# Kernel optimization log

Measured on AMD Instinct MI355X. Metric: run time of the kernel, lower is better.

Reference implementation:

```python
import jax, jax.numpy as jnp
import numpy as np

B, N, D, H = 8, 577, 768, 12
HD = D // H
SCALE = HD ** -0.5
LN_EPS = 1e-5


def layer_norm(x, w, b):
    mu = jnp.mean(x, -1, keepdims=True)
    var = jnp.mean((x - mu) ** 2, -1, keepdims=True)
    return (x - mu) * jax.lax.rsqrt(var + LN_EPS) * w + b


def wasserstein_distance_matmul(mean1, cov1, mean2, cov2):
    # all [B,H,N,hd]; returns [B,H,N,N]
    m1_2 = jnp.sum(mean1 ** 2, -1, keepdims=True)
    m2_2 = jnp.sum(mean2 ** 2, -1, keepdims=True)
    ret = -2.0 * jnp.einsum('bhnd,bhmd->bhnm', mean1, mean2) + m1_2 + jnp.swapaxes(m2_2, -1, -2)
    c1s = jnp.sqrt(jnp.clip(cov1, 1e-24))
    c2s = jnp.sqrt(jnp.clip(cov2, 1e-24))
    cov_ret = (-2.0 * jnp.einsum('bhnd,bhmd->bhnm', c1s, c2s)
               + jnp.sum(cov1, -1, keepdims=True)
               + jnp.swapaxes(jnp.sum(cov2, -1, keepdims=True), -1, -2))
    return ret + cov_ret


def setup_inputs() -> dict:
    key = jax.random.key(0)
    ks = jax.random.split(key, 20)
    s = 0.02
    return {
        'x_mean': jax.random.normal(ks[0], (B, N, D), jnp.float32),
        'x_cov': jax.random.normal(ks[1], (B, N, D), jnp.float32),
        'rel_pos_bias': jax.random.normal(ks[2], (1, H, N, N), jnp.float32),
        'norm1_w': jnp.ones((D,), jnp.float32),
        'norm1_b': jnp.zeros((D,), jnp.float32),
        'qkv_w': jax.random.normal(ks[3], (3 * D, D), jnp.float32) * s,
        'proj_w': jax.random.normal(ks[4], (D, D), jnp.float32) * s,
        'proj_b': jnp.zeros((D,), jnp.float32),
        'cov_proj_w': jax.random.normal(ks[5], (D, D), jnp.float32) * s,
        'cov_proj_b': jnp.zeros((D,), jnp.float32),
        'norm2_w': jnp.ones((D,), jnp.float32),
        'norm2_b': jnp.zeros((D,), jnp.float32),
        'fc1_w': jax.random.normal(ks[6], (4 * D, D), jnp.float32) * s,
        'fc1_b': jnp.zeros((4 * D,), jnp.float32),
        'fc2_w': jax.random.normal(ks[7], (D, 4 * D), jnp.float32) * s,
        'fc2_b': jnp.zeros((D,), jnp.float32),
        'gamma1': 0.1 * jnp.ones((D,), jnp.float32),
        'gamma2': 0.1 * jnp.ones((D,), jnp.float32),
    }


def _split_heads(t):
    # [B,N,3D] -> q,k,v each [B,H,N,hd]
    t = t.reshape(B, N, 3, H, HD).transpose(2, 0, 3, 1, 4)
    return t[0], t[1], t[2]


def attention(xm, xc, rel_pos_bias, qkv_w, proj_w, proj_b, cov_proj_w, cov_proj_b):
    qkv = xm @ qkv_w.T                                  # [B,N,3D]
    q, k, v = _split_heads(qkv)
    cov_qkv = jax.nn.elu(xc @ qkv_w.T) + 1.0            # same weights for cov stream
    cov_q, cov_k, cov_v = _split_heads(cov_qkv)
    q = q * SCALE
    attn = -wasserstein_distance_matmul(q, cov_q, k, cov_k)
    attn = jax.nn.sigmoid(attn + 1e-24)
    attn = jax.nn.softmax(attn + rel_pos_bias, axis=-1)  # [B,H,N,N]
    mean_ctx = jnp.einsum('bhnm,bhmd->bhnd', attn, v).transpose(0, 2, 1, 3).reshape(B, N, D)
    cov_ctx = jnp.einsum('bhnm,bhmd->bhnd', attn ** 2, cov_v).transpose(0, 2, 1, 3).reshape(B, N, D)
    mean_out = mean_ctx @ proj_w.T + proj_b
    cov_out = cov_ctx @ cov_proj_w.T + cov_proj_b
    return mean_out, cov_out


def mlp(x, fc1_w, fc1_b, fc2_w, fc2_b):
    h = jax.nn.gelu(x @ fc1_w.T + fc1_b, approximate=False)
    return h @ fc2_w.T + fc2_b


def reference(x_mean, x_cov, rel_pos_bias, norm1_w, norm1_b, qkv_w, proj_w, proj_b,
              cov_proj_w, cov_proj_b, norm2_w, norm2_b, fc1_w, fc1_b, fc2_w, fc2_b,
              gamma1, gamma2):
    mean, cov = attention(layer_norm(x_mean, norm1_w, norm1_b),
                          layer_norm(x_cov, norm1_w, norm1_b),
                          rel_pos_bias, qkv_w, proj_w, proj_b, cov_proj_w, cov_proj_b)
    x_mean = x_mean + gamma1 * mean
    fcm = gamma2 * mlp(layer_norm(x_mean, norm2_w, norm2_b), fc1_w, fc1_b, fc2_w, fc2_b)
    x_cov = x_cov + gamma1 * cov
    fcc = gamma2 * mlp(layer_norm(x_cov, norm2_w, norm2_b), fc1_w, fc1_b, fc2_w, fc2_b)
    return (x_mean + fcm, x_cov + fcc)
```

## Files before the change

kernel.cpp:

```cpp
#include <hip/hip_runtime.h>
#include <hip/hip_bf16.h>
#include <math.h>
#include <stdint.h>

typedef __bf16 bf16;
typedef __attribute__((ext_vector_type(8))) __bf16 bf16x8;
typedef __attribute__((ext_vector_type(4))) float f32x4;

typedef __attribute__((address_space(1))) void gas_void;
typedef __attribute__((address_space(3))) void las_void;

#define DEV __device__ __forceinline__

static constexpr int B_ = 8, N_ = 577, D_ = 768, H_ = 12;
static constexpr int M_ = B_ * N_;
static constexpr int MP_ = 4736;
static constexpr int NP_ = 640;
static constexpr int BH_ = B_ * H_;
static constexpr float SCALE_ = 0.125f;

DEV void async_cp16(const void* g, void* l) {
  __builtin_amdgcn_global_load_lds((gas_void*)g, (las_void*)l, 16, 0, 0);
}
DEV float fast_rcp(float x) { return __builtin_amdgcn_rcpf(x); }
DEV float elu1(float x) { return x > 0.0f ? x + 1.0f : __expf(x); }
DEV float fast_gelu(float x) {
  const float x2 = x * x;
  const float z = x * fmaf(0.0713548826f, x2, 1.5957691216f);
  return x * fast_rcp(1.0f + __expf(-z));
}

__global__ __launch_bounds__(256) void cvt6_kernel(
    const float* __restrict__ s0, const float* __restrict__ s1,
    const float* __restrict__ s2, const float* __restrict__ s3,
    const float* __restrict__ s4, const float* __restrict__ s5,
    bf16* __restrict__ d0, bf16* __restrict__ d1, bf16* __restrict__ d2,
    bf16* __restrict__ d3, bf16* __restrict__ d4, bf16* __restrict__ d5,
    int n0, int n1, int n2, int n3, int n4c, int n5) {
  const float* ss[6] = {s0, s1, s2, s3, s4, s5};
  bf16* dd[6] = {d0, d1, d2, d3, d4, d5};
  const int nn[6] = {n0, n1, n2, n3, n4c, n5};
  int bid = blockIdx.x;
  int seg = 0;
#pragma unroll 6
  for (int k = 0; k < 6; k++) {
    const int nb = (nn[k] + 255) >> 8;
    if (bid < nb) { seg = k; break; }
    bid -= nb;
  }
  const int i = bid * 256 + threadIdx.x;
  if (i < nn[seg]) {
    const float4 v = ((const float4*)ss[seg])[i];
    bf16 o[4] = {(bf16)v.x, (bf16)v.y, (bf16)v.z, (bf16)v.w};
    *(uint64_t*)(dd[seg] + (size_t)i * 4) = *(const uint64_t*)o;
  }
}

__global__ __launch_bounds__(256) void ln2_kernel(
    const float* __restrict__ x0, const float* __restrict__ x1,
    const float* __restrict__ w, const float* __restrict__ bp,
    bf16* __restrict__ out) {
  const int row = blockIdx.x;
  const int st = (int)(row >= M_);
  const int srow = row - st * M_;
  const float* xr = (st ? x1 : x0) + (size_t)srow * D_;
  const int t = threadIdx.x;
  float v0 = xr[t], v1 = xr[t + 256], v2 = xr[t + 512];
  float s = v0 + v1 + v2;
  float ss = v0 * v0 + v1 * v1 + v2 * v2;
#pragma unroll
  for (int m = 32; m >= 1; m >>= 1) {
    s += __shfl_down(s, m);
    ss += __shfl_down(ss, m);
  }
  __shared__ float red[8];
  if ((t & 63) == 0) { red[t >> 6] = s; red[4 + (t >> 6)] = ss; }
  __syncthreads();
  s = red[0] + red[1] + red[2] + red[3];
  ss = red[4] + red[5] + red[6] + red[7];
  const float mu = s * (1.0f / D_);
  float var = ss * (1.0f / D_) - mu * mu;
  var = fmaxf(var, 0.0f);
  const float rs = rsqrtf(var + 1e-5f);
  bf16* orow = out + ((size_t)st * MP_ + srow) * D_;
  orow[t]       = (bf16)((v0 - mu) * rs * w[t]       + bp[t]);
  orow[t + 256] = (bf16)((v1 - mu) * rs * w[t + 256] + bp[t + 256]);
  orow[t + 512] = (bf16)((v2 - mu) * rs * w[t + 512] + bp[t + 512]);
}

enum { EP_BF16 = 0, EP_PROJ = 1, EP_GELU = 2, EP_FC2 = 3 };

template <int EP, int K>
__global__ __launch_bounds__(256) void gemm_bt(
    const bf16* __restrict__ A, const bf16* __restrict__ W0,
    const bf16* __restrict__ W1, int Nn, int gx,
    const float* __restrict__ bias0, const float* __restrict__ bias1,
    const float* __restrict__ gamma,
    const float* __restrict__ resid0, const float* __restrict__ resid1,
    bf16* __restrict__ Cb, float* __restrict__ Cf0, float* __restrict__ Cf1) {
  __shared__ __align__(16) bf16 As[3][128 * 32];
  __shared__ __align__(16) bf16 Bs[3][128 * 32];
  const int nwg = gridDim.x;
  const int o = blockIdx.x;
  const int q = nwg >> 3, r = nwg & 7, xcd = o & 7;
  const int flat = (xcd < r ? xcd * (q + 1) : r * (q + 1) + (xcd - r) * q) + (o >> 3);
  const int bx = flat % gx, by = flat / gx;

  const int t = threadIdx.x;
  const int lane = t & 63, wv = t >> 6;
  const int ln = lane & 15, kg = lane >> 4;
  const int wr = wv >> 1, wc = wv & 1;
  const int s = (int)(by >= (MP_ / 128));
  const bf16* W = s ? W1 : W0;
  const size_t brow = (size_t)by * 128;
  const size_t bcol = (size_t)bx * 128;
  const int r0 = t >> 2, gsl = t & 3;
  const bf16* A0 = A + (brow + r0) * (size_t)K + gsl * 8;
  const bf16* A1 = A + (brow + r0 + 64) * (size_t)K + gsl * 8;
  const bf16* W0p = W + (bcol + r0) * (size_t)K + gsl * 8;
  const bf16* W1p = W + (bcol + r0 + 64) * (size_t)K + gsl * 8;

  auto stage = [&](int buf, int kk) {
    async_cp16(A0 + kk, &As[buf][(wv * 64) * 8]);
    async_cp16(A1 + kk, &As[buf][(256 + wv * 64) * 8]);
    async_cp16(W0p + kk, &Bs[buf][(wv * 64) * 8]);
    async_cp16(W1p + kk, &Bs[buf][(256 + wv * 64) * 8]);
  };

  f32x4 acc[4][4] = {};
  constexpr int nt = K >> 5;
  static_assert(nt % 3 == 0, "K/32 must be divisible by 3");
  stage(0, 0);
  stage(1, 32);
#pragma unroll 1
  for (int tb = 0; tb < nt; tb += 3) {
#pragma unroll
    for (int u = 0; u < 3; u++) {
      const int tt = tb + u;
      if (tt + 1 < nt) {
        asm volatile("s_waitcnt vmcnt(4)" ::: "memory");
      } else {
        asm volatile("s_waitcnt vmcnt(0)" ::: "memory");
      }
      __builtin_amdgcn_s_barrier();
      bf16x8 af[4], bfr[4];
#pragma unroll
      for (int i = 0; i < 4; i++)
        af[i] = *(const bf16x8*)&As[u][(wr * 64 + i * 16 + ln) * 32 + kg * 8];
#pragma unroll
      for (int j = 0; j < 4; j++)
        bfr[j] = *(const bf16x8*)&Bs[u][(wc * 64 + j * 16 + ln) * 32 + kg * 8];
#pragma unroll
      for (int i = 0; i < 4; i++)
#pragma unroll
        for (int j = 0; j < 4; j++)
          acc[i][j] = __builtin_amdgcn_mfma_f32_16x16x32_bf16(af[i], bfr[j], acc[i][j], 0, 0, 0);
      if (tt + 2 < nt) stage((u + 2) % 3, (tt + 2) * 32);
    }
  }

  const float* biasS = s ? bias1 : bias0;
  const float* residS = s ? resid1 : resid0;
  float* CfS = s ? Cf1 : Cf0;
#pragma unroll
  for (int i = 0; i < 4; i++) {
    const int rb = (int)brow + wr * 64 + i * 16 + kg * 4;
#pragma unroll
    for (int j = 0; j < 4; j++) {
      const int col = (int)bcol + wc * 64 + j * 16 + ln;
#pragma unroll
      for (int rr = 0; rr < 4; rr++) {
        const int row = rb + rr;
        float v = acc[i][j][rr];
        if (EP == EP_BF16) {
          Cb[(size_t)row * Nn + col] = (bf16)v;
        } else if (EP == EP_GELU) {
          v += biasS[col];
          Cb[(size_t)row * Nn + col] = (bf16)fast_gelu(v);
        } else {
          const int r2 = row - s * MP_;
          if (r2 < M_) {
            v += biasS[col];
            if (EP == EP_PROJ) {
              CfS[(size_t)r2 * Nn + col] = residS[(size_t)r2 * Nn + col] + gamma[col] * v;
            } else {
              CfS[(size_t)r2 * Nn + col] += gamma[col] * v;
            }
          }
        }
      }
    }
  }
}

__global__ __launch_bounds__(256) void prep_kernel(
    const bf16* __restrict__ qm, const bf16* __restrict__ qc,
    bf16* __restrict__ Qcat, bf16* __restrict__ Kcat,
    bf16* __restrict__ Vt, bf16* __restrict__ CVt,
    float* __restrict__ rowt, float* __restrict__ colt) {
  const int n0 = blockIdx.x * 64;
  const int h = blockIdx.y, b = blockIdx.z;
  const int bh = b * H_ + h;
  const int t = threadIdx.x;
  const int nl = t >> 2, c = t & 3;
  const int n = n0 + nl;
  const bool valid = n < N_;
  __shared__ bf16 vts[64][72], cvts[64][72];
  float q2 = 0.f, cqs = 0.f, k2 = 0.f, cks = 0.f;
  bf16 qo[16], sqo[16], ko[16], sko[16];
  if (valid) {
    const size_t ro = (size_t)(b * N_ + n) * 2304 + h * 64 + c * 16;
#pragma unroll
    for (int half = 0; half < 2; half++) {
      bf16x8 qv8 = *(const bf16x8*)(qm + ro + half * 8);
      bf16x8 kv8 = *(const bf16x8*)(qm + ro + 768 + half * 8);
      bf16x8 vv8 = *(const bf16x8*)(qm + ro + 1536 + half * 8);
      bf16x8 cq8 = *(const bf16x8*)(qc + ro + half * 8);
      bf16x8 ck8 = *(const bf16x8*)(qc + ro + 768 + half * 8);
      bf16x8 cv8 = *(const bf16x8*)(qc + ro + 1536 + half * 8);
#pragma unroll
      for (int i = 0; i < 8; i++) {
        const int d = half * 8 + i;
        float qv = (float)qv8[i] * SCALE_;
        float kv = (float)kv8[i];
        float cq1 = elu1((float)cq8[i]);
        float ck1 = elu1((float)ck8[i]);
        q2 += qv * qv; cqs += cq1; k2 += kv * kv; cks += ck1;
        qo[d] = (bf16)qv; sqo[d] = (bf16)sqrtf(fmaxf(cq1, 1e-24f));
        ko[d] = (bf16)kv; sko[d] = (bf16)sqrtf(fmaxf(ck1, 1e-24f));
        vts[nl][c * 16 + d] = vv8[i];
        cvts[nl][c * 16 + d] = (bf16)elu1((float)cv8[i]);
      }
    }
  } else {
#pragma unroll
    for (int d = 0; d < 16; d++) {
      qo[d] = (bf16)0.f; sqo[d] = (bf16)0.f; ko[d] = (bf16)0.f; sko[d] = (bf16)0.f;
      vts[nl][c * 16 + d] = (bf16)0.f; cvts[nl][c * 16 + d] = (bf16)0.f;
    }
  }
  {
    bf16* qrow = Qcat + ((size_t)bh * NP_ + n) * 128;
    bf16* krow = Kcat + ((size_t)bh * NP_ + n) * 128;
#pragma unroll
    for (int d = 0; d < 16; d++) {
      qrow[c * 16 + d] = qo[d];
      qrow[64 + c * 16 + d] = sqo[d];
      krow[c * 16 + d] = ko[d];
      krow[64 + c * 16 + d] = sko[d];
    }
  }
  float rt = q2 + cqs, ct = k2 + cks;
  rt += __shfl_xor(rt, 1); rt += __shfl_xor(rt, 2);
  ct += __shfl_xor(ct, 1); ct += __shfl_xor(ct, 2);
  if (c == 0) { rowt[(size_t)bh * NP_ + n] = rt; colt[(size_t)bh * NP_ + n] = ct; }
  __syncthreads();
  const int drow = t >> 2;
  const size_t vb = ((size_t)bh * 64 + drow) * NP_ + n0 + c * 16;
#pragma unroll
  for (int i = 0; i < 16; i++) {
    Vt[vb + i] = vts[c * 16 + i][drow];
    CVt[vb + i] = cvts[c * 16 + i][drow];
  }
}

__global__ __launch_bounds__(256) void attn_kernel(
    const bf16* __restrict__ Qcat, const bf16* __restrict__ Kcat,
    const bf16* __restrict__ Vt, const bf16* __restrict__ CVt,
    const float* __restrict__ rowt, const float* __restrict__ colt,
    const bf16* __restrict__ bias,
    bf16* __restrict__ ctxm, bf16* __restrict__ ctxc) {
  const int id = blockIdx.x;
  const int xcd = id & 7, slot = id >> 3;
  const int g = xcd + 8 * (slot / 10);
  const int it = slot % 10;
  const int b = g / H_, h = g % H_;
  const int bh = g;
  const int i0 = it * 64;
  const int t = threadIdx.x;
  const int lane = t & 63, w = t >> 6;
  const int ln = lane & 15, kg = lane >> 4;
  __shared__ __align__(16) bf16 Ks[64 * 128];
  __shared__ __align__(16) bf16 Vs[64 * 64];
  __shared__ __align__(16) bf16 CVs[64 * 64];
  __shared__ __align__(16) bf16 Ps[64 * 72];

  const bf16* Qg = Qcat + (size_t)bh * NP_ * 128;
  const bf16* Kg = Kcat + (size_t)bh * NP_ * 128;
  const bf16* Vg = Vt + (size_t)bh * 64 * NP_;
  const bf16* CVg = CVt + (size_t)bh * 64 * NP_;

#pragma unroll
  for (int qq = 0; qq < 4; qq++) {
    const int idx = qq * 256 + t;
    const int row = idx >> 4, sl = idx & 15;
    async_cp16(Qg + (size_t)(i0 + row) * 128 + ((sl ^ (row & 7)) * 8),
               &Ks[(qq * 256 + w * 64) * 8]);
  }
  __syncthreads();
  bf16x8 aq[4];
  {
    const int row = w * 16 + ln;
#pragma unroll
    for (int kc = 0; kc < 4; kc++) {
      const int slot2 = kc * 4 + kg;
      aq[kc] = *(const bf16x8*)&Ks[row * 128 + ((slot2 ^ (row & 7)) * 8)];
    }
  }
  float rt[4];
#pragma unroll
  for (int r = 0; r < 4; r++) rt[r] = rowt[(size_t)bh * NP_ + i0 + w * 16 + kg * 4 + r];

  f32x4 accm[4] = {}, accc[4] = {};
  float den[4] = {0.f, 0.f, 0.f, 0.f};
  const int igb = i0 + w * 16 + kg * 4;

  for (int jt = 0; jt < 10; jt++) {
    const int j0 = jt * 64;
    __syncthreads();
#pragma unroll
    for (int qq = 0; qq < 4; qq++) {
      const int idx = qq * 256 + t;
      const int row = idx >> 4, sl = idx & 15;
      async_cp16(Kg + (size_t)(j0 + row) * 128 + ((sl ^ (row & 7)) * 8),
                 &Ks[(qq * 256 + w * 64) * 8]);
    }
#pragma unroll
    for (int qq = 0; qq < 2; qq++) {
      const int idx = qq * 256 + t;
      const int row = idx >> 3, sl = idx & 7;
      async_cp16(Vg + (size_t)row * NP_ + j0 + ((sl ^ (row & 7)) * 8),
                 &Vs[(qq * 256 + w * 64) * 8]);
      async_cp16(CVg + (size_t)row * NP_ + j0 + ((sl ^ (row & 7)) * 8),
                 &CVs[(qq * 256 + w * 64) * 8]);
    }
    float bb[4][4], ctb[4];
#pragma unroll
    for (int js = 0; js < 4; js++) {
      const int jg = j0 + js * 16 + ln;
      const int jc = jg < N_ ? jg : N_ - 1;
      ctb[js] = colt[(size_t)bh * NP_ + jg];
#pragma unroll
      for (int r = 0; r < 4; r++) {
        const int ic = (igb + r) < N_ ? (igb + r) : N_ - 1;
        bb[js][r] = (float)bias[((size_t)h * N_ + ic) * N_ + jc];
      }
    }
    __syncthreads();
#pragma unroll
    for (int js = 0; js < 4; js++) {
      f32x4 sv = {};
#pragma unroll
      for (int kc = 0; kc < 4; kc++) {
        const int row = js * 16 + ln;
        const int slot2 = kc * 4 + kg;
        bf16x8 bk = *(const bf16x8*)&Ks[row * 128 + ((slot2 ^ (row & 7)) * 8)];
        sv = __builtin_amdgcn_mfma_f32_16x16x32_bf16(aq[kc], bk, sv, 0, 0, 0);
      }
      const int jg = j0 + js * 16 + ln;
#pragma unroll
      for (int r = 0; r < 4; r++) {
        const float S = 2.0f * sv[r] - rt[r] - ctb[js];
        const float sig = fast_rcp(1.0f + __expf(-S));
        float e = __expf(sig + bb[js][r]);
        if (jg >= N_) e = 0.0f;
        const bf16 eb = (bf16)e;
        den[r] += (float)eb;
        Ps[(w * 16 + kg * 4 + r) * 72 + js * 16 + ln] = eb;
      }
    }
#pragma unroll
    for (int ks = 0; ks < 2; ks++) {
      const int prow = w * 16 + ln;
      bf16x8 pa = *(const bf16x8*)&Ps[prow * 72 + ks * 32 + kg * 8];
      bf16x8 p2a;
#pragma unroll
      for (int i = 0; i < 8; i++) {
        const float pf = (float)pa[i];
        p2a[i] = (bf16)(pf * pf);
      }
#pragma unroll
      for (int nt = 0; nt < 4; nt++) {
        const int vrow = nt * 16 + ln;
        const int slot2 = ks * 4 + kg;
        bf16x8 vb = *(const bf16x8*)&Vs[vrow * 64 + ((slot2 ^ (vrow & 7)) * 8)];
        bf16x8 cvb = *(const bf16x8*)&CVs[vrow * 64 + ((slot2 ^ (vrow & 7)) * 8)];
        accm[nt] = __builtin_amdgcn_mfma_f32_16x16x32_bf16(pa, vb, accm[nt], 0, 0, 0);
        accc[nt] = __builtin_amdgcn_mfma_f32_16x16x32_bf16(p2a, cvb, accc[nt], 0, 0, 0);
      }
    }
  }
#pragma unroll
  for (int r = 0; r < 4; r++) {
    float d = den[r];
    d += __shfl_xor(d, 1); d += __shfl_xor(d, 2);
    d += __shfl_xor(d, 4); d += __shfl_xor(d, 8);
    den[r] = d;
  }
#pragma unroll
  for (int r = 0; r < 4; r++) {
    const int ig = i0 + w * 16 + kg * 4 + r;
    if (ig < N_) {
      const float inv = fast_rcp(den[r]);
      const float inv2 = inv * inv;
      const size_t base = (size_t)(b * N_ + ig) * D_ + h * 64;
#pragma unroll
      for (int nt = 0; nt < 4; nt++) {
        ctxm[base + nt * 16 + ln] = (bf16)(accm[nt][r] * inv);
        ctxc[base + nt * 16 + ln] = (bf16)(accc[nt][r] * inv2);
      }
    }
  }
}

extern "C" void kernel_launch(void* const* d_in, const int* in_sizes, int n_in,
                              void* d_out, int out_size, void* d_ws, size_t ws_size,
                              hipStream_t stream) {
  const float* x_mean = (const float*)d_in[0];
  const float* x_cov  = (const float*)d_in[1];
  const float* rpb    = (const float*)d_in[2];
  const float* n1w    = (const float*)d_in[3];
  const float* n1b    = (const float*)d_in[4];
  const float* qkvw   = (const float*)d_in[5];
  const float* projw  = (const float*)d_in[6];
  const float* projb  = (const float*)d_in[7];
  const float* cprojw = (const float*)d_in[8];
  const float* cprojb = (const float*)d_in[9];
  const float* n2w    = (const float*)d_in[10];
  const float* n2b    = (const float*)d_in[11];
  const float* fc1w   = (const float*)d_in[12];
  const float* fc1b   = (const float*)d_in[13];
  const float* fc2w   = (const float*)d_in[14];
  const float* fc2b   = (const float*)d_in[15];
  const float* g1     = (const float*)d_in[16];
  const float* g2     = (const float*)d_in[17];
  (void)in_sizes; (void)n_in; (void)out_size; (void)ws_size;

  char* ws = (char*)d_ws;
  size_t off = 0;
  auto take = [&](size_t bytes) {
    char* p = ws + off;
    off += (bytes + 255) & ~(size_t)255;
    return p;
  };
  bf16* wq   = (bf16*)take((size_t)2304 * 768 * 2);
  bf16* wp   = (bf16*)take((size_t)768 * 768 * 2);
  bf16* wcp  = (bf16*)take((size_t)768 * 768 * 2);
  bf16* wf1  = (bf16*)take((size_t)3072 * 768 * 2);
  bf16* wf2  = (bf16*)take((size_t)768 * 3072 * 2);
  bf16* xln  = (bf16*)take((size_t)2 * MP_ * 768 * 2);
  char* R    = take((size_t)2 * MP_ * 3072 * 2);
  bf16* qkvb = (bf16*)R;
  bf16* hbuf = (bf16*)R;
  bf16* biasb = (bf16*)(R + (size_t)2 * MP_ * 2304 * 2);
  bf16* Qcat = (bf16*)take((size_t)BH_ * NP_ * 128 * 2);
  bf16* Kcat = (bf16*)take((size_t)BH_ * NP_ * 128 * 2);
  bf16* Vt   = (bf16*)take((size_t)BH_ * 64 * NP_ * 2);
  bf16* CVt  = (bf16*)take((size_t)BH_ * 64 * NP_ * 2);
  float* rowt = (float*)take((size_t)BH_ * NP_ * 4);
  float* colt = (float*)take((size_t)BH_ * NP_ * 4);
  bf16* ctx  = (bf16*)take((size_t)2 * MP_ * 768 * 2);

  float* outm = (float*)d_out;
  float* outc = outm + (size_t)M_ * D_;

  {
    const int c0 = 2304 * 768 / 4, c1 = 768 * 768 / 4, c2 = 768 * 768 / 4;
    const int c3 = 3072 * 768 / 4, c4 = 768 * 3072 / 4, c5 = H_ * N_ * N_ / 4;
    const int nb = ((c0 + 255) >> 8) + ((c1 + 255) >> 8) + ((c2 + 255) >> 8) +
                   ((c3 + 255) >> 8) + ((c4 + 255) >> 8) + ((c5 + 255) >> 8);
    cvt6_kernel<<<nb, 256, 0, stream>>>(qkvw, projw, cprojw, fc1w, fc2w, rpb,
                                        wq, wp, wcp, wf1, wf2, biasb,
                                        c0, c1, c2, c3, c4, c5);
  }
  ln2_kernel<<<2 * M_, 256, 0, stream>>>(x_mean, x_cov, n1w, n1b, xln);
  gemm_bt<EP_BF16, 768><<<18 * 74, 256, 0, stream>>>(xln, wq, wq, 2304, 18,
      nullptr, nullptr, nullptr, nullptr, nullptr, qkvb, nullptr, nullptr);
  prep_kernel<<<dim3(10, 12, 8), 256, 0, stream>>>(
      qkvb, qkvb + (size_t)MP_ * 2304, Qcat, Kcat, Vt, CVt, rowt, colt);
  attn_kernel<<<960, 256, 0, stream>>>(Qcat, Kcat, Vt, CVt, rowt, colt, biasb,
                                       ctx, ctx + (size_t)MP_ * 768);
  gemm_bt<EP_PROJ, 768><<<6 * 74, 256, 0, stream>>>(ctx, wp, wcp, 768, 6,
      projb, cprojb, g1, x_mean, x_cov, nullptr, outm, outc);
  ln2_kernel<<<2 * M_, 256, 0, stream>>>(outm, outc, n2w, n2b, xln);
  gemm_bt<EP_GELU, 768><<<24 * 74, 256, 0, stream>>>(xln, wf1, wf1, 3072, 24,
      fc1b, fc1b, nullptr, nullptr, nullptr, hbuf, nullptr, nullptr);
  gemm_bt<EP_FC2, 3072><<<6 * 74, 256, 0, stream>>>(hbuf, wf2, wf2, 768, 6,
      fc2b, fc2b, g2, nullptr, nullptr, nullptr, outm, outc);
}
```

Before: 370.4 us.

## Fuse QKV prep into GEMM epilogue and split-K the FC2 GEMM

Replaces the QKV GEMM plus separate prep kernel with a gemm_qkv kernel whose epilogue writes the scaled Q, K, sqrt-ELU covariance parts, transposed V/CV and row/col norm sums straight into attention layouts. Norms are accumulated with atomics, and a small pad kernel zeroes the padded rows and the norm buffers beforehand. This removes the intermediate qkv buffer round-trip and one launch. The FC2 GEMM is split into two K halves with atomicAdd accumulation, with bias added only by the first half, which doubles the grid for better occupancy. The cost is atomic traffic, nondeterministic summation order, and strided transposed V stores from the GEMM epilogue.

```diff
diff --git a/kernel.cpp b/kernel.cpp
--- a/kernel.cpp
+++ b/kernel.cpp
@@ -56,6 +56,26 @@
   }
 }
 
+__global__ __launch_bounds__(256) void pad_kernel(
+    bf16* __restrict__ Qcat, bf16* __restrict__ Kcat,
+    bf16* __restrict__ Vt, bf16* __restrict__ CVt,
+    float* __restrict__ rowt, float* __restrict__ colt) {
+  const int bh = blockIdx.x;
+  const int t = threadIdx.x;
+  bf16* q = Qcat + ((size_t)bh * NP_ + N_) * 128;
+  bf16* k = Kcat + ((size_t)bh * NP_ + N_) * 128;
+  for (int i = t; i < (NP_ - N_) * 128; i += 256) { q[i] = (bf16)0.f; k[i] = (bf16)0.f; }
+  for (int i = t; i < 64 * (NP_ - N_); i += 256) {
+    const int d = i / (NP_ - N_), c = i % (NP_ - N_);
+    Vt[((size_t)bh * 64 + d) * NP_ + N_ + c] = (bf16)0.f;
+    CVt[((size_t)bh * 64 + d) * NP_ + N_ + c] = (bf16)0.f;
+  }
+  for (int i = t; i < NP_; i += 256) {
+    rowt[(size_t)bh * NP_ + i] = 0.f;
+    colt[(size_t)bh * NP_ + i] = 0.f;
+  }
+}
+
 __global__ __launch_bounds__(256) void ln2_kernel(
     const float* __restrict__ x0, const float* __restrict__ x1,
     const float* __restrict__ w, const float* __restrict__ bp,
@@ -88,12 +108,12 @@
   orow[t + 512] = (bf16)((v2 - mu) * rs * w[t + 512] + bp[t + 512]);
 }
 
-enum { EP_BF16 = 0, EP_PROJ = 1, EP_GELU = 2, EP_FC2 = 3 };
-
-template <int EP, int K>
+enum { EP_PROJ = 1, EP_GELU = 2, EP_FC2 = 3 };
+
+template <int EP, int K, int KS>
 __global__ __launch_bounds__(256) void gemm_bt(
     const bf16* __restrict__ A, const bf16* __restrict__ W0,
-    const bf16* __restrict__ W1, int Nn, int gx,
+    const bf16* __restrict__ W1, int Nn, int gx, int gyh, int koff,
     const float* __restrict__ bias0, const float* __restrict__ bias1,
     const float* __restrict__ gamma,
     const float* __restrict__ resid0, const float* __restrict__ resid1,
@@ -104,7 +124,10 @@
   const int o = blockIdx.x;
   const int q = nwg >> 3, r = nwg & 7, xcd = o & 7;
   const int flat = (xcd < r ? xcd * (q + 1) : r * (q + 1) + (xcd - r) * q) + (o >> 3);
-  const int bx = flat % gx, by = flat / gx;
+  const int bx = flat % gx;
+  int by = flat / gx;
+  int kof = koff;
+  if (by >= gyh) { by -= gyh; kof += K; }
 
   const int t = threadIdx.x;
   const int lane = t & 63, wv = t >> 6;
@@ -115,10 +138,10 @@
   const size_t brow = (size_t)by * 128;
   const size_t bcol = (size_t)bx * 128;
   const int r0 = t >> 2, gsl = t & 3;
-  const bf16* A0 = A + (brow + r0) * (size_t)K + gsl * 8;
-  const bf16* A1 = A + (brow + r0 + 64) * (size_t)K + gsl * 8;
-  const bf16* W0p = W + (bcol + r0) * (size_t)K + gsl * 8;
-  const bf16* W1p = W + (bcol + r0 + 64) * (size_t)K + gsl * 8;
+  const bf16* A0 = A + (brow + r0) * (size_t)KS + kof + gsl * 8;
+  const bf16* A1 = A + (brow + r0 + 64) * (size_t)KS + kof + gsl * 8;
+  const bf16* W0p = W + (bcol + r0) * (size_t)KS + kof + gsl * 8;
+  const bf16* W1p = W + (bcol + r0 + 64) * (size_t)KS + kof + gsl * 8;
 
   auto stage = [&](int buf, int kk) {
     async_cp16(A0 + kk, &As[buf][(wv * 64) * 8]);
@@ -172,19 +195,18 @@
       for (int rr = 0; rr < 4; rr++) {
         const int row = rb + rr;
         float v = acc[i][j][rr];
-        if (EP == EP_BF16) {
-          Cb[(size_t)row * Nn + col] = (bf16)v;
-        } else if (EP == EP_GELU) {
+        if (EP == EP_GELU) {
           v += biasS[col];
           Cb[(size_t)row * Nn + col] = (bf16)fast_gelu(v);
         } else {
           const int r2 = row - s * MP_;
           if (r2 < M_) {
-            v += biasS[col];
             if (EP == EP_PROJ) {
+              v += biasS[col];
               CfS[(size_t)r2 * Nn + col] = residS[(size_t)r2 * Nn + col] + gamma[col] * v;
             } else {
-              CfS[(size_t)r2 * Nn + col] += gamma[col] * v;
+              if (kof == koff) v += biasS[col];
+              atomicAdd(&CfS[(size_t)r2 * Nn + col], gamma[col] * v);
             }
           }
         }
@@ -193,74 +215,143 @@
   }
 }
 
-__global__ __launch_bounds__(256) void prep_kernel(
-    const bf16* __restrict__ qm, const bf16* __restrict__ qc,
+__global__ __launch_bounds__(256) void gemm_qkv(
+    const bf16* __restrict__ A, const bf16* __restrict__ W,
     bf16* __restrict__ Qcat, bf16* __restrict__ Kcat,
     bf16* __restrict__ Vt, bf16* __restrict__ CVt,
     float* __restrict__ rowt, float* __restrict__ colt) {
-  const int n0 = blockIdx.x * 64;
-  const int h = blockIdx.y, b = blockIdx.z;
-  const int bh = b * H_ + h;
+  constexpr int K = 768, Nn = 2304, gx = 18;
+  __shared__ __align__(16) bf16 As[3][128 * 32];
+  __shared__ __align__(16) bf16 Bs[3][128 * 32];
+  const int nwg = gridDim.x;
+  const int o = blockIdx.x;
+  const int q = nwg >> 3, r = nwg & 7, xcd = o & 7;
+  const int flat = (xcd < r ? xcd * (q + 1) : r * (q + 1) + (xcd - r) * q) + (o >> 3);
+  const int bx = flat % gx, by = flat / gx;
+
   const int t = threadIdx.x;
-  const int nl = t >> 2, c = t & 3;
-  const int n = n0 + nl;
-  const bool valid = n < N_;
-  __shared__ bf16 vts[64][72], cvts[64][72];
-  float q2 = 0.f, cqs = 0.f, k2 = 0.f, cks = 0.f;
-  bf16 qo[16], sqo[16], ko[16], sko[16];
-  if (valid) {
-    const size_t ro = (size_t)(b * N_ + n) * 2304 + h * 64 + c * 16;
-#pragma unroll
-    for (int half = 0; half < 2; half++) {
-      bf16x8 qv8 = *(const bf16x8*)(qm + ro + half * 8);
-      bf16x8 kv8 = *(const bf16x8*)(qm + ro + 768 + half * 8);
-      bf16x8 vv8 = *(const bf16x8*)(qm + ro + 1536 + half * 8);
-      bf16x8 cq8 = *(const bf16x8*)(qc + ro + half * 8);
-      bf16x8 ck8 = *(const bf16x8*)(qc + ro + 768 + half * 8);
-      bf16x8 cv8 = *(const bf16x8*)(qc + ro + 1536 + half * 8);
-#pragma unroll
-      for (int i = 0; i < 8; i++) {
-        const int d = half * 8 + i;
-        float qv = (float)qv8[i] * SCALE_;
-        float kv = (float)kv8[i];
-        float cq1 = elu1((float)cq8[i]);
-        float ck1 = elu1((float)ck8[i]);
-        q2 += qv * qv; cqs += cq1; k2 += kv * kv; cks += ck1;
-        qo[d] = (bf16)qv; sqo[d] = (bf16)sqrtf(fmaxf(cq1, 1e-24f));
-        ko[d] = (bf16)kv; sko[d] = (bf16)sqrtf(fmaxf(ck1, 1e-24f));
-        vts[nl][c * 16 + d] = vv8[i];
-        cvts[nl][c * 16 + d] = (bf16)elu1((float)cv8[i]);
-      }
-    }
-  } else {
-#pragma unroll
-    for (int d = 0; d < 16; d++) {
-      qo[d] = (bf16)0.f; sqo[d] = (bf16)0.f; ko[d] = (bf16)0.f; sko[d] = (bf16)0.f;
-      vts[nl][c * 16 + d] = (bf16)0.f; cvts[nl][c * 16 + d] = (bf16)0.f;
-    }
-  }
-  {
-    bf16* qrow = Qcat + ((size_t)bh * NP_ + n) * 128;
-    bf16* krow = Kcat + ((size_t)bh * NP_ + n) * 128;
-#pragma unroll
-    for (int d = 0; d < 16; d++) {
-      qrow[c * 16 + d] = qo[d];
-      qrow[64 + c * 16 + d] = sqo[d];
-      krow[c * 16 + d] = ko[d];
-      krow[64 + c * 16 + d] = sko[d];
-    }
-  }
-  float rt = q2 + cqs, ct = k2 + cks;
-  rt += __shfl_xor(rt, 1); rt += __shfl_xor(rt, 2);
-  ct += __shfl_xor(ct, 1); ct += __shfl_xor(ct, 2);
-  if (c == 0) { rowt[(size_t)bh * NP_ + n] = rt; colt[(size_t)bh * NP_ + n] = ct; }
-  __syncthreads();
-  const int drow = t >> 2;
-  const size_t vb = ((size_t)bh * 64 + drow) * NP_ + n0 + c * 16;
-#pragma unroll
-  for (int i = 0; i < 16; i++) {
-    Vt[vb + i] = vts[c * 16 + i][drow];
-    CVt[vb + i] = cvts[c * 16 + i][drow];
+  const int lane = t & 63, wv = t >> 6;
+  const int ln = lane & 15, kg = lane >> 4;
+  const int wr = wv >> 1, wc = wv & 1;
+  const int s = (int)(by >= (MP_ / 128));
+  const size_t brow = (size_t)by * 128;
+  const size_t bcol = (size_t)bx * 128;
+  const int r0 = t >> 2, gsl = t & 3;
+  const bf16* A0 = A + (brow + r0) * (size_t)K + gsl * 8;
+  const bf16* A1 = A + (brow + r0 + 64) * (size_t)K + gsl * 8;
+  const bf16* W0p = W + (bcol + r0) * (size_t)K + gsl * 8;
+  const bf16* W1p = W + (bcol + r0 + 64) * (size_t)K + gsl * 8;
+
+  auto stage = [&](int buf, int kk) {
+    async_cp16(A0 + kk, &As[buf][(wv * 64) * 8]);
+    async_cp16(A1 + kk, &As[buf][(256 + wv * 64) * 8]);
+    async_cp16(W0p + kk, &Bs[buf][(wv * 64) * 8]);
+    async_cp16(W1p + kk, &Bs[buf][(256 + wv * 64) * 8]);
+  };
+
+  f32x4 acc[4][4] = {};
+  constexpr int nt = K >> 5;
+  stage(0, 0);
+  stage(1, 32);
+#pragma unroll 1
+  for (int tb = 0; tb < nt; tb += 3) {
+#pragma unroll
+    for (int u = 0; u < 3; u++) {
+      const int tt = tb + u;
+      if (tt + 1 < nt) {
+        asm volatile("s_waitcnt vmcnt(4)" ::: "memory");
+      } else {
+        asm volatile("s_waitcnt vmcnt(0)" ::: "memory");
+      }
+      __builtin_amdgcn_s_barrier();
+      bf16x8 af[4], bfr[4];
+#pragma unroll
+      for (int i = 0; i < 4; i++)
+        af[i] = *(const bf16x8*)&As[u][(wr * 64 + i * 16 + ln) * 32 + kg * 8];
+#pragma unroll
+      for (int j = 0; j < 4; j++)
+        bfr[j] = *(const bf16x8*)&Bs[u][(wc * 64 + j * 16 + ln) * 32 + kg * 8];
+#pragma unroll
+      for (int i = 0; i < 4; i++)
+#pragma unroll
+        for (int j = 0; j < 4; j++)
+          acc[i][j] = __builtin_amdgcn_mfma_f32_16x16x32_bf16(af[i], bfr[j], acc[i][j], 0, 0, 0);
+      if (tt + 2 < nt) stage((u + 2) % 3, (tt + 2) * 32);
+    }
+  }
+
+  const int colbase = (int)bcol + wc * 64;
+  const int sect = colbase / 768;
+  const int hd = (colbase % 768) / 64;
+#pragma unroll
+  for (int i = 0; i < 4; i++) {
+#pragma unroll
+    for (int rr = 0; rr < 4; rr++) {
+      const int rowl = (int)brow + wr * 64 + i * 16 + kg * 4 + rr;
+      const int r2 = rowl - s * MP_;
+      const bool vld = r2 < M_;
+      const int bb2 = vld ? (r2 / N_) : 0;
+      const int n = vld ? (r2 - bb2 * N_) : 0;
+      const int bh = bb2 * H_ + hd;
+      float red = 0.f;
+      if (s == 0) {
+        if (sect == 0) {
+          bf16* qr = Qcat + ((size_t)bh * NP_ + n) * 128;
+#pragma unroll
+          for (int j = 0; j < 4; j++) {
+            const float v = acc[i][j][rr] * SCALE_;
+            red += v * v;
+            if (vld) qr[j * 16 + ln] = (bf16)v;
+          }
+        } else if (sect == 1) {
+          bf16* kr = Kcat + ((size_t)bh * NP_ + n) * 128;
+#pragma unroll
+          for (int j = 0; j < 4; j++) {
+            const float v = acc[i][j][rr];
+            red += v * v;
+            if (vld) kr[j * 16 + ln] = (bf16)v;
+          }
+        } else {
+#pragma unroll
+          for (int j = 0; j < 4; j++) {
+            if (vld) Vt[((size_t)bh * 64 + j * 16 + ln) * NP_ + n] = (bf16)acc[i][j][rr];
+          }
+        }
+      } else {
+        if (sect == 0) {
+          bf16* qr = Qcat + ((size_t)bh * NP_ + n) * 128 + 64;
+#pragma unroll
+          for (int j = 0; j < 4; j++) {
+            const float e = elu1(acc[i][j][rr]);
+            red += e;
+            if (vld) qr[j * 16 + ln] = (bf16)sqrtf(fmaxf(e, 1e-24f));
+          }
+        } else if (sect == 1) {
+          bf16* kr = Kcat + ((size_t)bh * NP_ + n) * 128 + 64;
+#pragma unroll
+          for (int j = 0; j < 4; j++) {
+            const float e = elu1(acc[i][j][rr]);
+            red += e;
+            if (vld) kr[j * 16 + ln] = (bf16)sqrtf(fmaxf(e, 1e-24f));
+          }
+        } else {
+#pragma unroll
+          for (int j = 0; j < 4; j++) {
+            if (vld) CVt[((size_t)bh * 64 + j * 16 + ln) * NP_ + n] = (bf16)elu1(acc[i][j][rr]);
+          }
+        }
+      }
+      if (sect < 2) {
+        red += __shfl_xor(red, 1);
+        red += __shfl_xor(red, 2);
+        red += __shfl_xor(red, 4);
+        red += __shfl_xor(red, 8);
+        if (ln == 0 && vld) {
+          float* tgt = (sect == 0) ? rowt : colt;
+          atomicAdd(&tgt[(size_t)bh * NP_ + n], red);
+        }
+      }
+    }
   }
 }
 
@@ -450,7 +541,6 @@
   bf16* wf2  = (bf16*)take((size_t)768 * 3072 * 2);
   bf16* xln  = (bf16*)take((size_t)2 * MP_ * 768 * 2);
   char* R    = take((size_t)2 * MP_ * 3072 * 2);
-  bf16* qkvb = (bf16*)R;
   bf16* hbuf = (bf16*)R;
   bf16* biasb = (bf16*)(R + (size_t)2 * MP_ * 2304 * 2);
   bf16* Qcat = (bf16*)take((size_t)BH_ * NP_ * 128 * 2);
@@ -474,17 +564,15 @@
                                         c0, c1, c2, c3, c4, c5);
   }
   ln2_kernel<<<2 * M_, 256, 0, stream>>>(x_mean, x_cov, n1w, n1b, xln);
-  gemm_bt<EP_BF16, 768><<<18 * 74, 256, 0, stream>>>(xln, wq, wq, 2304, 18,
-      nullptr, nullptr, nullptr, nullptr, nullptr, qkvb, nullptr, nullptr);
-  prep_kernel<<<dim3(10, 12, 8), 256, 0, stream>>>(
-      qkvb, qkvb + (size_t)MP_ * 2304, Qcat, Kcat, Vt, CVt, rowt, colt);
+  pad_kernel<<<BH_, 256, 0, stream>>>(Qcat, Kcat, Vt, CVt, rowt, colt);
+  gemm_qkv<<<18 * 74, 256, 0, stream>>>(xln, wq, Qcat, Kcat, Vt, CVt, rowt, colt);
   attn_kernel<<<960, 256, 0, stream>>>(Qcat, Kcat, Vt, CVt, rowt, colt, biasb,
                                        ctx, ctx + (size_t)MP_ * 768);
-  gemm_bt<EP_PROJ, 768><<<6 * 74, 256, 0, stream>>>(ctx, wp, wcp, 768, 6,
+  gemm_bt<EP_PROJ, 768, 768><<<6 * 74, 256, 0, stream>>>(ctx, wp, wcp, 768, 6, 74, 0,
       projb, cprojb, g1, x_mean, x_cov, nullptr, outm, outc);
   ln2_kernel<<<2 * M_, 256, 0, stream>>>(outm, outc, n2w, n2b, xln);
-  gemm_bt<EP_GELU, 768><<<24 * 74, 256, 0, stream>>>(xln, wf1, wf1, 3072, 24,
+  gemm_bt<EP_GELU, 768, 768><<<24 * 74, 256, 0, stream>>>(xln, wf1, wf1, 3072, 24, 74, 0,
       fc1b, fc1b, nullptr, nullptr, nullptr, hbuf, nullptr, nullptr);
-  gemm_bt<EP_FC2, 3072><<<6 * 74, 256, 0, stream>>>(hbuf, wf2, wf2, 768, 6,
+  gemm_bt<EP_FC2, 1536, 3072><<<6 * 148, 256, 0, stream>>>(hbuf, wf2, wf2, 768, 6, 74, 0,
       fc2b, fc2b, g2, nullptr, nullptr, nullptr, outm, outc);
 }
```

New measurement: 455.9 us. +23.1%, slower.

## Double-buffer K, V and CV tiles in attention kernel to prefetch next tile

Applied to the files above, without the earlier changes.

The attention kernel now uses two LDS buffers each for the K, V and CV tiles. Loads for tile j+1 are issued at the start of iteration j, and a single barrier sits at the end of each iteration instead of two around the load. The aim is to hide global-to-LDS copy latency behind the QK and PV MFMA work and to cut barriers per iteration. In exchange the kernel needs roughly twice the LDS, which can lower the number of resident blocks per CU.

```diff
diff --git a/kernel.cpp b/kernel.cpp
--- a/kernel.cpp
+++ b/kernel.cpp
@@ -280,9 +280,9 @@
   const int t = threadIdx.x;
   const int lane = t & 63, w = t >> 6;
   const int ln = lane & 15, kg = lane >> 4;
-  __shared__ __align__(16) bf16 Ks[64 * 128];
-  __shared__ __align__(16) bf16 Vs[64 * 64];
-  __shared__ __align__(16) bf16 CVs[64 * 64];
+  __shared__ __align__(16) bf16 Ks[2][64 * 128];
+  __shared__ __align__(16) bf16 Vs[2][64 * 64];
+  __shared__ __align__(16) bf16 CVs[2][64 * 64];
   __shared__ __align__(16) bf16 Ps[64 * 72];
 
   const bf16* Qg = Qcat + (size_t)bh * NP_ * 128;
@@ -290,13 +290,36 @@
   const bf16* Vg = Vt + (size_t)bh * 64 * NP_;
   const bf16* CVg = CVt + (size_t)bh * 64 * NP_;
 
+  auto stageK = [&](int buf, int j0) {
+#pragma unroll
+    for (int qq = 0; qq < 4; qq++) {
+      const int idx = qq * 256 + t;
+      const int row = idx >> 4, sl = idx & 15;
+      async_cp16(Kg + (size_t)(j0 + row) * 128 + ((sl ^ (row & 7)) * 8),
+                 &Ks[buf][(qq * 256 + w * 64) * 8]);
+    }
+  };
+  auto stageV = [&](int buf, int j0) {
+#pragma unroll
+    for (int qq = 0; qq < 2; qq++) {
+      const int idx = qq * 256 + t;
+      const int row = idx >> 3, sl = idx & 7;
+      async_cp16(Vg + (size_t)row * NP_ + j0 + ((sl ^ (row & 7)) * 8),
+                 &Vs[buf][(qq * 256 + w * 64) * 8]);
+      async_cp16(CVg + (size_t)row * NP_ + j0 + ((sl ^ (row & 7)) * 8),
+                 &CVs[buf][(qq * 256 + w * 64) * 8]);
+    }
+  };
+
 #pragma unroll
   for (int qq = 0; qq < 4; qq++) {
     const int idx = qq * 256 + t;
     const int row = idx >> 4, sl = idx & 15;
     async_cp16(Qg + (size_t)(i0 + row) * 128 + ((sl ^ (row & 7)) * 8),
-               &Ks[(qq * 256 + w * 64) * 8]);
-  }
+               &Ks[0][(qq * 256 + w * 64) * 8]);
+  }
+  stageK(1, 0);
+  stageV(0, 0);
   __syncthreads();
   bf16x8 aq[4];
   {
@@ -304,12 +327,13 @@
 #pragma unroll
     for (int kc = 0; kc < 4; kc++) {
       const int slot2 = kc * 4 + kg;
-      aq[kc] = *(const bf16x8*)&Ks[row * 128 + ((slot2 ^ (row & 7)) * 8)];
+      aq[kc] = *(const bf16x8*)&Ks[0][row * 128 + ((slot2 ^ (row & 7)) * 8)];
     }
   }
   float rt[4];
 #pragma unroll
   for (int r = 0; r < 4; r++) rt[r] = rowt[(size_t)bh * NP_ + i0 + w * 16 + kg * 4 + r];
+  __syncthreads();
 
   f32x4 accm[4] = {}, accc[4] = {};
   float den[4] = {0.f, 0.f, 0.f, 0.f};
@@ -317,22 +341,11 @@
 
   for (int jt = 0; jt < 10; jt++) {
     const int j0 = jt * 64;
-    __syncthreads();
-#pragma unroll
-    for (int qq = 0; qq < 4; qq++) {
-      const int idx = qq * 256 + t;
-      const int row = idx >> 4, sl = idx & 15;
-      async_cp16(Kg + (size_t)(j0 + row) * 128 + ((sl ^ (row & 7)) * 8),
-                 &Ks[(qq * 256 + w * 64) * 8]);
-    }
-#pragma unroll
-    for (int qq = 0; qq < 2; qq++) {
-      const int idx = qq * 256 + t;
-      const int row = idx >> 3, sl = idx & 7;
-      async_cp16(Vg + (size_t)row * NP_ + j0 + ((sl ^ (row & 7)) * 8),
-                 &Vs[(qq * 256 + w * 64) * 8]);
-      async_cp16(CVg + (size_t)row * NP_ + j0 + ((sl ^ (row & 7)) * 8),
-                 &CVs[(qq * 256 + w * 64) * 8]);
+    const int kc2 = (jt + 1) & 1;
+    const int vc2 = jt & 1;
+    if (jt + 1 < 10) {
+      stageK(jt & 1, j0 + 64);
+      stageV((jt + 1) & 1, j0 + 64);
     }
     float bb[4][4], ctb[4];
 #pragma unroll
@@ -346,7 +359,6 @@
         bb[js][r] = (float)bias[((size_t)h * N_ + ic) * N_ + jc];
       }
     }
-    __syncthreads();
 #pragma unroll
     for (int js = 0; js < 4; js++) {
       f32x4 sv = {};
@@ -354,7 +366,7 @@
       for (int kc = 0; kc < 4; kc++) {
         const int row = js * 16 + ln;
         const int slot2 = kc * 4 + kg;
-        bf16x8 bk = *(const bf16x8*)&Ks[row * 128 + ((slot2 ^ (row & 7)) * 8)];
+        bf16x8 bk = *(const bf16x8*)&Ks[kc2][row * 128 + ((slot2 ^ (row & 7)) * 8)];
         sv = __builtin_amdgcn_mfma_f32_16x16x32_bf16(aq[kc], bk, sv, 0, 0, 0);
       }
       const int jg = j0 + js * 16 + ln;
@@ -383,12 +395,13 @@
       for (int nt = 0; nt < 4; nt++) {
         const int vrow = nt * 16 + ln;
         const int slot2 = ks * 4 + kg;
-        bf16x8 vb = *(const bf16x8*)&Vs[vrow * 64 + ((slot2 ^ (vrow & 7)) * 8)];
-        bf16x8 cvb = *(const bf16x8*)&CVs[vrow * 64 + ((slot2 ^ (vrow & 7)) * 8)];
+        bf16x8 vb = *(const bf16x8*)&Vs[vc2][vrow * 64 + ((slot2 ^ (vrow & 7)) * 8)];
+        bf16x8 cvb = *(const bf16x8*)&CVs[vc2][vrow * 64 + ((slot2 ^ (vrow & 7)) * 8)];
         accm[nt] = __builtin_amdgcn_mfma_f32_16x16x32_bf16(pa, vb, accm[nt], 0, 0, 0);
         accc[nt] = __builtin_amdgcn_mfma_f32_16x16x32_bf16(p2a, cvb, accc[nt], 0, 0, 0);
       }
     }
+    __syncthreads();
   }
 #pragma unroll
   for (int r = 0; r < 4; r++) {
```

New measurement: 371.6 us. No clear change (+0.3%).
